# Kernel optimization log

Hardware: AMD Instinct MI355X
Metric: run time of the kernel (lower is better)

Reference implementation:

```python
import jax, jax.numpy as jnp
import numpy as np

# Scalar quantization params (QLinear __init__ args)
FEATURE_BITWIDTH = 8
WEIGHT_BITWIDTH = 8
INPUT_ZERO_POINT = -3
OUTPUT_ZERO_POINT = -5
INPUT_SCALE = 0.05
OUTPUT_SCALE = 0.1
QMIN = -(1 << (FEATURE_BITWIDTH - 1))   # -128
QMAX = (1 << (FEATURE_BITWIDTH - 1)) - 1  # 127

M, K, N = 8192, 4096, 4096


def float_to_fixed_point(x, bitwidth):
    """Represent x (0 < x < 1) as int_scale * 2^-frac_bits with int_scale
    in [2^(bitwidth-2), 2^(bitwidth-1)) (mantissa fits in signed `bitwidth` bits)."""
    frac_bits = (bitwidth - 1 - jnp.ceil(jnp.log2(x))).astype(jnp.int32)
    int_scale = jnp.round(x * jnp.exp2(frac_bits.astype(jnp.float32))).astype(jnp.int32)
    return int_scale, frac_bits


def setup_inputs() -> dict:
    key = jax.random.key(0)
    k1, k2, k3, k4 = jax.random.split(key, 4)
    qinput = jax.random.randint(k1, (M, K), -128, 128, dtype=jnp.int8)
    qweight = jax.random.randint(k2, (N, K), -128, 128, dtype=jnp.int8)
    qbias = jax.random.randint(k3, (N,), -(1 << 16), 1 << 16, dtype=jnp.int32)
    # per-output-channel weight scale; keeps folded scale in (0, 1)
    weight_scale = jax.random.uniform(k4, (N,), jnp.float32, 0.002, 0.02)
    return {"qinput": qinput, "qweight": qweight, "qbias": qbias,
            "weight_scale": weight_scale}


def reference(qinput, qweight, qbias, weight_scale):
    w32 = qweight.astype(jnp.int32)                      # [N, K]
    # Qbias' = qbias - sum_k(qweight) * Zin  (bias shift folding input zero point)
    shifted_qbias = qbias - w32.sum(axis=1) * INPUT_ZERO_POINT  # [N]
    # int32 GEMM: [M, K] @ [K, N] + bias
    acc = qinput.astype(jnp.int32) @ w32.T + shifted_qbias[None, :]  # [M, N]
    # fixed-point requantization: (acc * int_scale) >> frac_bits + Zout
    folded_scale = INPUT_SCALE * weight_scale / OUTPUT_SCALE         # [N], in (0,1)
    int_scale, frac_bits = float_to_fixed_point(folded_scale, FEATURE_BITWIDTH)
    # widen to int64 for the multiply so the (acc * int_scale) product cannot wrap
    prod = acc.astype(jnp.int64) * int_scale.astype(jnp.int64)[None, :]
    scaled = jnp.right_shift(prod, frac_bits.astype(jnp.int64)[None, :])  # arithmetic >>
    out = scaled + OUTPUT_ZERO_POINT
    return jnp.clip(out, QMIN, QMAX).astype(jnp.int8)
```

## Files before the change

### kernel.cpp

```cpp
#include <hip/hip_runtime.h>
#include <cstdint>
#include <cstddef>

#define M_DIM 8192
#define N_DIM 4096
#define K_DIM 4096

#define BM 128
#define BN 128
#define BK 128

typedef int int32x4 __attribute__((ext_vector_type(4)));


typedef __attribute__((address_space(1))) const void* gas_cptr;
typedef __attribute__((address_space(3))) void* las_ptr;

__device__ __forceinline__ void async_copy16(const void* g, void* l) {
    __builtin_amdgcn_global_load_lds((gas_cptr)g, (las_ptr)l, 16, 0, 0);
}

__device__ __forceinline__ int32x4 pack16(const int* p) {
    const int32x4* v = (const int32x4*)p;
    int32x4 w0 = v[0], w1 = v[1], w2 = v[2], w3 = v[3];
    int32x4 r;
    r.x = (w0.x & 0xFF) | ((w0.y & 0xFF) << 8) | ((w0.z & 0xFF) << 16) | (w0.w << 24);
    r.y = (w1.x & 0xFF) | ((w1.y & 0xFF) << 8) | ((w1.z & 0xFF) << 16) | (w1.w << 24);
    r.z = (w2.x & 0xFF) | ((w2.y & 0xFF) << 8) | ((w2.z & 0xFF) << 16) | (w2.w << 24);
    r.w = (w3.x & 0xFF) | ((w3.y & 0xFF) << 8) | ((w3.z & 0xFF) << 16) | (w3.w << 24);
    return r;
}

__global__ void ql_detect_kernel(const int* a, const int* b, int* ws) {
    int t = threadIdx.x;
    int fa = 0, fb = 0;
    for (int i = t; i < 4096; i += 64) {
        int va = a[i]; if (va > 127 || va < -128) fa = 1;
        int vb = b[i]; if (vb > 127 || vb < -128) fb = 1;
    }
    unsigned long long ba = __ballot(fa);
    unsigned long long bb = __ballot(fb);
    if (t == 0) { ws[0] = ba ? 1 : 0; ws[1] = bb ? 1 : 0; }
}

__global__ __launch_bounds__(256)
void ql_pack_kernel(const void* src, int* dst, const int* ws, int flag_idx, long ndw) {
    const int f8 = __builtin_amdgcn_readfirstlane(ws[flag_idx]);
    const long stride = (long)gridDim.x * 256;
    for (long c = (long)blockIdx.x * 256 + threadIdx.x; c < ndw; c += stride) {
        if (f8) {
            dst[c] = ((const int*)src)[c];
        } else {
            int32x4 v = ((const int32x4*)src)[c];
            dst[c] = (v.x & 0xFF) | ((v.y & 0xFF) << 8) | ((v.z & 0xFF) << 16) | (v.w << 24);
        }
    }
}

__global__ void ql_prep8_kernel(const int8_t* w8, const int* qbias,
                                const float* wscale, int* ws) {
    const int lane = threadIdx.x & 63;
    const int wid  = threadIdx.x >> 6;
    const int n = blockIdx.x * 4 + wid;

    const int32x4* row = (const int32x4*)(w8 + (size_t)n * K_DIM);
    int s = 0;
    for (int c = lane; c < K_DIM / 16; c += 64) {
        int32x4 v = row[c];
#pragma unroll
        for (int j = 0; j < 4; ++j) {
            int w = (j == 0) ? v.x : (j == 1) ? v.y : (j == 2) ? v.z : v.w;
            s += (int)(int8_t)(w) + (int)(int8_t)(w >> 8)
               + (int)(int8_t)(w >> 16) + (w >> 24);
        }
    }
#pragma unroll
    for (int off = 32; off > 0; off >>= 1) s += __shfl_down(s, off, 64);

    if (lane == 0) {
        ws[16 + n] = qbias[n] + 3 * s;
        float folded = (0.05f * wscale[n]) / 0.1f;
        int fbits = (int)(7.0f - ceilf(log2f(folded)));
        int isc = (int)rintf(folded * exp2f((float)fbits));
        ws[16 + N_DIM + n] = isc;
        ws[16 + 2 * N_DIM + n] = fbits;
    }
}

__global__ void ql_prep_kernel(const void* wptr, const int* qbias,
                               const float* wscale, int* ws) {
    const int lane = threadIdx.x & 63;
    const int wid  = threadIdx.x >> 6;
    const int n = blockIdx.x * 4 + wid;
    const int b8 = __builtin_amdgcn_readfirstlane(ws[1]);

    int s = 0;
    if (b8) {
        const int32x4* row = (const int32x4*)((const int8_t*)wptr + (size_t)n * K_DIM);
        for (int c = lane; c < K_DIM / 16; c += 64) {
            int32x4 v = row[c];
#pragma unroll
            for (int j = 0; j < 4; ++j) {
                int w = (j == 0) ? v.x : (j == 1) ? v.y : (j == 2) ? v.z : v.w;
                s += (int)(int8_t)(w) + (int)(int8_t)(w >> 8)
                   + (int)(int8_t)(w >> 16) + (w >> 24);
            }
        }
    } else {
        const int32x4* row = (const int32x4*)((const int*)wptr + (size_t)n * K_DIM);
        for (int c = lane; c < K_DIM / 4; c += 64) {
            int32x4 v = row[c];
            s += v.x + v.y + v.z + v.w;
        }
    }
#pragma unroll
    for (int off = 32; off > 0; off >>= 1) s += __shfl_down(s, off, 64);

    if (lane == 0) {
        ws[16 + n] = qbias[n] + 3 * s;
        float folded = (0.05f * wscale[n]) / 0.1f;
        int fbits = (int)(7.0f - ceilf(log2f(folded)));
        int isc = (int)rintf(folded * exp2f((float)fbits));
        ws[16 + N_DIM + n] = isc;
        ws[16 + 2 * N_DIM + n] = fbits;
    }
}

__device__ __forceinline__ void ql_epilogue(int32x4 acc[4][4], const int* ws,
                                            int* out, int bm, int bn,
                                            int wm, int wn, int qm, int qh) {
    const int* qb  = ws + 16;
    const int* isc = ws + 16 + N_DIM;
    const int* fbt = ws + 16 + 2 * N_DIM;
#pragma unroll
    for (int j = 0; j < 4; ++j) {
        const int n_g = bn * BN + wn + j * 16 + qm;
        const int b0 = qb[n_g];
        const int s0 = isc[n_g];
        const int f0 = fbt[n_g];
#pragma unroll
        for (int i = 0; i < 4; ++i) {
            const int m_base = bm * BM + wm + i * 16 + qh * 4;
#pragma unroll
            for (int r = 0; r < 4; ++r) {
                int v = ((r == 0) ? acc[i][j].x : (r == 1) ? acc[i][j].y
                        : (r == 2) ? acc[i][j].z : acc[i][j].w) + b0;
                long long p = (long long)v * (long long)s0;
                int o = (int)(p >> f0) - 5;
                o = o < -128 ? -128 : (o > 127 ? 127 : o);
                out[(size_t)(m_base + r) * N_DIM + n_g] = o;
            }
        }
    }
}

__global__ __launch_bounds__(256)
void ql_gemm_kernel(const int8_t* aptr, const int8_t* bptr, const int* ws, int* out) {
    __shared__ int32x4 Als[BM * BK / 16];
    __shared__ int32x4 Bls[BN * BK / 16];

    const int t    = threadIdx.x;
    const int lane = t & 63;
    const int wid  = t >> 6;
    const int bn = blockIdx.x;
    const int bm = blockIdx.y;

    const int wm = (wid >> 1) * 64;
    const int wn = (wid & 1) * 64;
    const int qm = lane & 15;
    const int qh = lane >> 4;

    int32x4 acc[4][4] = {};

    for (int kt = 0; kt < K_DIM / BK; ++kt) {
        __syncthreads();
        const int k0 = kt * BK;
#pragma unroll
        for (int r = 0; r < 4; ++r) {
            const int c    = r * 256 + t;
            const int row  = c >> 3;
            const int colg = (c & 7) ^ (row & 7);
            const size_t offA = (size_t)(bm * BM + row) * K_DIM + k0 + colg * 16;
            const size_t offB = (size_t)(bn * BN + row) * K_DIM + k0 + colg * 16;
            async_copy16(aptr + offA, &Als[c]);
            async_copy16(bptr + offB, &Bls[c]);
        }
        __syncthreads();

#pragma unroll
        for (int s = 0; s < 2; ++s) {
            const int colk = s * 4 + qh;
            int32x4 af[4], bf[4];
#pragma unroll
            for (int i = 0; i < 4; ++i) {
                const int ra = wm + i * 16 + qm;
                const int rb = wn + i * 16 + qm;
                af[i] = Als[ra * 8 + (colk ^ (ra & 7))];
                bf[i] = Bls[rb * 8 + (colk ^ (rb & 7))];
            }
#pragma unroll
            for (int i = 0; i < 4; ++i)
#pragma unroll
                for (int j = 0; j < 4; ++j)
                    acc[i][j] = __builtin_amdgcn_mfma_i32_16x16x64_i8(
                        af[i], bf[j], acc[i][j], 0, 0, 0);
        }
    }
    ql_epilogue(acc, ws, out, bm, bn, wm, wn, qm, qh);
}

__global__ __launch_bounds__(256)
void ql_gemm_fb_kernel(const void* aptr, const void* bptr, const int* ws, int* out) {
    __shared__ int32x4 Als[BM * BK / 16];
    __shared__ int32x4 Bls[BN * BK / 16];

    const int a8 = __builtin_amdgcn_readfirstlane(ws[0]);
    const int b8 = __builtin_amdgcn_readfirstlane(ws[1]);

    const int t    = threadIdx.x;
    const int lane = t & 63;
    const int wid  = t >> 6;
    const int bn = blockIdx.x;
    const int bm = blockIdx.y;

    const int wm = (wid >> 1) * 64;
    const int wn = (wid & 1) * 64;
    const int qm = lane & 15;
    const int qh = lane >> 4;

    int32x4 acc[4][4] = {};

    for (int kt = 0; kt < K_DIM / BK; ++kt) {
        __syncthreads();
        const int k0 = kt * BK;
#pragma unroll
        for (int r = 0; r < 4; ++r) {
            const int c    = r * 256 + t;
            const int row  = c >> 3;
            const int colg = (c & 7) ^ (row & 7);
            const size_t offA = (size_t)(bm * BM + row) * K_DIM + k0 + colg * 16;
            const size_t offB = (size_t)(bn * BN + row) * K_DIM + k0 + colg * 16;
            if (a8) async_copy16((const int8_t*)aptr + offA, &Als[c]);
            else    Als[c] = pack16((const int*)aptr + offA);
            if (b8) async_copy16((const int8_t*)bptr + offB, &Bls[c]);
            else    Bls[c] = pack16((const int*)bptr + offB);
        }
        __syncthreads();

#pragma unroll
        for (int s = 0; s < 2; ++s) {
            const int colk = s * 4 + qh;
            int32x4 af[4], bf[4];
#pragma unroll
            for (int i = 0; i < 4; ++i) {
                const int ra = wm + i * 16 + qm;
                const int rb = wn + i * 16 + qm;
                af[i] = Als[ra * 8 + (colk ^ (ra & 7))];
                bf[i] = Bls[rb * 8 + (colk ^ (rb & 7))];
            }
#pragma unroll
            for (int i = 0; i < 4; ++i)
#pragma unroll
                for (int j = 0; j < 4; ++j)
                    acc[i][j] = __builtin_amdgcn_mfma_i32_16x16x64_i8(
                        af[i], bf[j], acc[i][j], 0, 0, 0);
        }
    }
    ql_epilogue(acc, ws, out, bm, bn, wm, wn, qm, qh);
}

extern "C" void kernel_launch(void* const* d_in, const int* in_sizes, int n_in,
                              void* d_out, int out_size, void* d_ws, size_t ws_size,
                              hipStream_t stream) {
    const void* qin    = d_in[0];
    const void* qwt    = d_in[1];
    const int* qbias   = (const int*)d_in[2];
    const float* wscal = (const float*)d_in[3];
    int* ws  = (int*)d_ws;
    int* out = (int*)d_out;

    hipLaunchKernelGGL(ql_detect_kernel, dim3(1), dim3(64), 0, stream,
                       (const int*)qin, (const int*)qwt, ws);

    const size_t need = 65536 + (size_t)M_DIM * K_DIM + (size_t)N_DIM * K_DIM;
    if (ws_size >= need) {
        int8_t* a8 = (int8_t*)d_ws + 65536;
        int8_t* w8 = a8 + (size_t)M_DIM * K_DIM;
        const long ndwA = (long)M_DIM * K_DIM / 4;
        const long ndwW = (long)N_DIM * K_DIM / 4;
        hipLaunchKernelGGL(ql_pack_kernel, dim3((unsigned)(ndwW / (256 * 4))), dim3(256),
                           0, stream, qwt, (int*)w8, ws, 1, ndwW);
        hipLaunchKernelGGL(ql_pack_kernel, dim3((unsigned)(ndwA / (256 * 4))), dim3(256),
                           0, stream, qin, (int*)a8, ws, 0, ndwA);
        hipLaunchKernelGGL(ql_prep8_kernel, dim3(N_DIM / 4), dim3(256), 0, stream,
                           w8, qbias, wscal, ws);
        hipLaunchKernelGGL(ql_gemm_kernel, dim3(N_DIM / BN, M_DIM / BM), dim3(256), 0, stream,
                           a8, w8, ws, out);
    } else {
        hipLaunchKernelGGL(ql_prep_kernel, dim3(N_DIM / 4), dim3(256), 0, stream,
                           qwt, qbias, wscal, ws);
        hipLaunchKernelGGL(ql_gemm_fb_kernel, dim3(N_DIM / BN, M_DIM / BM), dim3(256), 0, stream,
                           qin, qwt, ws, out);
    }
}
```

Baseline: 440.1 us.

## Double-buffer GEMM LDS tiles, stage epilogue stores through LDS, merge pack kernels

The main int8 GEMM now double-buffers its A and B tiles in LDS. Global-to-LDS async copies for the next K tile are issued before the MFMAs on the current tile, and one barrier per iteration replaces two. The epilogue writes requantized values into a per-wave LDS scratch area and then stores 16-byte vectors along N, replacing scattered 4-byte column stores to the large int32 output. The two pack launches are merged into one kernel covering both inputs, which saves a launch. Doubling LDS per block to 64KB may lower the number of resident blocks per CU.

```diff
diff --git a/kernel.cpp b/kernel.cpp
--- a/kernel.cpp
+++ b/kernel.cpp
@@ -44,15 +44,26 @@
 }
 
 __global__ __launch_bounds__(256)
-void ql_pack_kernel(const void* src, int* dst, const int* ws, int flag_idx, long ndw) {
-    const int f8 = __builtin_amdgcn_readfirstlane(ws[flag_idx]);
+void ql_pack2_kernel(const void* asrc, const void* bsrc, int* adst, int* bdst,
+                     const int* ws, long ndwA, long ndwW) {
+    const int fa = __builtin_amdgcn_readfirstlane(ws[0]);
+    const int fb = __builtin_amdgcn_readfirstlane(ws[1]);
+    const long total = ndwA + ndwW;
     const long stride = (long)gridDim.x * 256;
-    for (long c = (long)blockIdx.x * 256 + threadIdx.x; c < ndw; c += stride) {
-        if (f8) {
-            dst[c] = ((const int*)src)[c];
+    for (long c = (long)blockIdx.x * 256 + threadIdx.x; c < total; c += stride) {
+        if (c < ndwA) {
+            if (fa) adst[c] = ((const int*)asrc)[c];
+            else {
+                int32x4 v = ((const int32x4*)asrc)[c];
+                adst[c] = (v.x & 0xFF) | ((v.y & 0xFF) << 8) | ((v.z & 0xFF) << 16) | (v.w << 24);
+            }
         } else {
-            int32x4 v = ((const int32x4*)src)[c];
-            dst[c] = (v.x & 0xFF) | ((v.y & 0xFF) << 8) | ((v.z & 0xFF) << 16) | (v.w << 24);
+            long d = c - ndwA;
+            if (fb) bdst[d] = ((const int*)bsrc)[d];
+            else {
+                int32x4 v = ((const int32x4*)bsrc)[d];
+                bdst[d] = (v.x & 0xFF) | ((v.y & 0xFF) << 8) | ((v.z & 0xFF) << 16) | (v.w << 24);
+            }
         }
     }
 }
@@ -126,38 +137,14 @@
     }
 }
 
-__device__ __forceinline__ void ql_epilogue(int32x4 acc[4][4], const int* ws,
-                                            int* out, int bm, int bn,
-                                            int wm, int wn, int qm, int qh) {
-    const int* qb  = ws + 16;
-    const int* isc = ws + 16 + N_DIM;
-    const int* fbt = ws + 16 + 2 * N_DIM;
-#pragma unroll
-    for (int j = 0; j < 4; ++j) {
-        const int n_g = bn * BN + wn + j * 16 + qm;
-        const int b0 = qb[n_g];
-        const int s0 = isc[n_g];
-        const int f0 = fbt[n_g];
-#pragma unroll
-        for (int i = 0; i < 4; ++i) {
-            const int m_base = bm * BM + wm + i * 16 + qh * 4;
-#pragma unroll
-            for (int r = 0; r < 4; ++r) {
-                int v = ((r == 0) ? acc[i][j].x : (r == 1) ? acc[i][j].y
-                        : (r == 2) ? acc[i][j].z : acc[i][j].w) + b0;
-                long long p = (long long)v * (long long)s0;
-                int o = (int)(p >> f0) - 5;
-                o = o < -128 ? -128 : (o > 127 ? 127 : o);
-                out[(size_t)(m_base + r) * N_DIM + n_g] = o;
-            }
-        }
-    }
+__device__ __forceinline__ int acc_elem(const int32x4& a, int r) {
+    return (r == 0) ? a.x : (r == 1) ? a.y : (r == 2) ? a.z : a.w;
 }
 
 __global__ __launch_bounds__(256)
 void ql_gemm_kernel(const int8_t* aptr, const int8_t* bptr, const int* ws, int* out) {
-    __shared__ int32x4 Als[BM * BK / 16];
-    __shared__ int32x4 Bls[BN * BK / 16];
+    __shared__ int32x4 Ab[2][BM * BK / 16];
+    __shared__ int32x4 Bb[2][BN * BK / 16];
 
     const int t    = threadIdx.x;
     const int lane = t & 63;
@@ -172,20 +159,32 @@
 
     int32x4 acc[4][4] = {};
 
+#pragma unroll
+    for (int r = 0; r < 4; ++r) {
+        const int c    = r * 256 + t;
+        const int row  = c >> 3;
+        const int colg = (c & 7) ^ (row & 7);
+        async_copy16(aptr + (size_t)(bm * BM + row) * K_DIM + colg * 16, &Ab[0][c]);
+        async_copy16(bptr + (size_t)(bn * BN + row) * K_DIM + colg * 16, &Bb[0][c]);
+    }
+
+    int cur = 0;
     for (int kt = 0; kt < K_DIM / BK; ++kt) {
         __syncthreads();
-        const int k0 = kt * BK;
-#pragma unroll
-        for (int r = 0; r < 4; ++r) {
-            const int c    = r * 256 + t;
-            const int row  = c >> 3;
-            const int colg = (c & 7) ^ (row & 7);
-            const size_t offA = (size_t)(bm * BM + row) * K_DIM + k0 + colg * 16;
-            const size_t offB = (size_t)(bn * BN + row) * K_DIM + k0 + colg * 16;
-            async_copy16(aptr + offA, &Als[c]);
-            async_copy16(bptr + offB, &Bls[c]);
-        }
-        __syncthreads();
+        if (kt + 1 < K_DIM / BK) {
+            const int k1 = (kt + 1) * BK;
+            const int nxt = cur ^ 1;
+#pragma unroll
+            for (int r = 0; r < 4; ++r) {
+                const int c    = r * 256 + t;
+                const int row  = c >> 3;
+                const int colg = (c & 7) ^ (row & 7);
+                async_copy16(aptr + (size_t)(bm * BM + row) * K_DIM + k1 + colg * 16,
+                             &Ab[nxt][c]);
+                async_copy16(bptr + (size_t)(bn * BN + row) * K_DIM + k1 + colg * 16,
+                             &Bb[nxt][c]);
+            }
+        }
 
 #pragma unroll
         for (int s = 0; s < 2; ++s) {
@@ -195,8 +194,8 @@
             for (int i = 0; i < 4; ++i) {
                 const int ra = wm + i * 16 + qm;
                 const int rb = wn + i * 16 + qm;
-                af[i] = Als[ra * 8 + (colk ^ (ra & 7))];
-                bf[i] = Bls[rb * 8 + (colk ^ (rb & 7))];
+                af[i] = Ab[cur][ra * 8 + (colk ^ (ra & 7))];
+                bf[i] = Bb[cur][rb * 8 + (colk ^ (rb & 7))];
             }
 #pragma unroll
             for (int i = 0; i < 4; ++i)
@@ -205,8 +204,43 @@
                     acc[i][j] = __builtin_amdgcn_mfma_i32_16x16x64_i8(
                         af[i], bf[j], acc[i][j], 0, 0, 0);
         }
-    }
-    ql_epilogue(acc, ws, out, bm, bn, wm, wn, qm, qh);
+        cur ^= 1;
+    }
+
+    __syncthreads();
+    const int* qb  = ws + 16;
+    const int* isc = ws + 16 + N_DIM;
+    const int* fbt = ws + 16 + 2 * N_DIM;
+
+    int* sc  = (int*)&Ab[0][0];
+    int* wsc = sc + wid * 1088;
+
+#pragma unroll
+    for (int i = 0; i < 4; ++i) {
+#pragma unroll
+        for (int j = 0; j < 4; ++j) {
+            const int n_g = bn * BN + wn + j * 16 + qm;
+            const int b0 = qb[n_g];
+            const int s0 = isc[n_g];
+            const int f0 = fbt[n_g];
+#pragma unroll
+            for (int r = 0; r < 4; ++r) {
+                int v = acc_elem(acc[i][j], r) + b0;
+                long long p = (long long)v * (long long)s0;
+                int o = (int)(p >> f0) - 5;
+                o = o < -128 ? -128 : (o > 127 ? 127 : o);
+                wsc[(qh * 4 + r) * 68 + j * 16 + qm] = o;
+            }
+        }
+#pragma unroll
+        for (int p4 = 0; p4 < 4; ++p4) {
+            const int lr = p4 * 4 + qh;
+            int32x4 vv = *(const int32x4*)&wsc[lr * 68 + qm * 4];
+            const size_t g = (size_t)(bm * BM + wm + i * 16 + lr) * N_DIM
+                           + bn * BN + wn + qm * 4;
+            *(int32x4*)(out + g) = vv;
+        }
+    }
 }
 
 __global__ __launch_bounds__(256)
@@ -266,7 +300,29 @@
                         af[i], bf[j], acc[i][j], 0, 0, 0);
         }
     }
-    ql_epilogue(acc, ws, out, bm, bn, wm, wn, qm, qh);
+
+    const int* qb  = ws + 16;
+    const int* isc = ws + 16 + N_DIM;
+    const int* fbt = ws + 16 + 2 * N_DIM;
+#pragma unroll
+    for (int j = 0; j < 4; ++j) {
+        const int n_g = bn * BN + wn + j * 16 + qm;
+        const int b0 = qb[n_g];
+        const int s0 = isc[n_g];
+        const int f0 = fbt[n_g];
+#pragma unroll
+        for (int i = 0; i < 4; ++i) {
+            const int m_base = bm * BM + wm + i * 16 + qh * 4;
+#pragma unroll
+            for (int r = 0; r < 4; ++r) {
+                int v = acc_elem(acc[i][j], r) + b0;
+                long long p = (long long)v * (long long)s0;
+                int o = (int)(p >> f0) - 5;
+                o = o < -128 ? -128 : (o > 127 ? 127 : o);
+                out[(size_t)(m_base + r) * N_DIM + n_g] = o;
+            }
+        }
+    }
 }
 
 extern "C" void kernel_launch(void* const* d_in, const int* in_sizes, int n_in,
@@ -288,10 +344,9 @@
         int8_t* w8 = a8 + (size_t)M_DIM * K_DIM;
         const long ndwA = (long)M_DIM * K_DIM / 4;
         const long ndwW = (long)N_DIM * K_DIM / 4;
-        hipLaunchKernelGGL(ql_pack_kernel, dim3((unsigned)(ndwW / (256 * 4))), dim3(256),
-                           0, stream, qwt, (int*)w8, ws, 1, ndwW);
-        hipLaunchKernelGGL(ql_pack_kernel, dim3((unsigned)(ndwA / (256 * 4))), dim3(256),
-                           0, stream, qin, (int*)a8, ws, 0, ndwA);
+        hipLaunchKernelGGL(ql_pack2_kernel, dim3((unsigned)((ndwA + ndwW) / (256 * 4))),
+                           dim3(256), 0, stream,
+                           qin, qwt, (int*)a8, (int*)w8, ws, ndwA, ndwW);
         hipLaunchKernelGGL(ql_prep8_kernel, dim3(N_DIM / 4), dim3(256), 0, stream,
                            w8, qbias, wscal, ws);
         hipLaunchKernelGGL(ql_gemm_kernel, dim3(N_DIM / BN, M_DIM / BM), dim3(256), 0, stream,
```

New measurement: 449.0 us. 2.0% more time.
